# Kernel optimization log

Measured on AMD Instinct MI355X. Metric: run time of the kernel, lower is better.

The kernel has to match this reference:

```python
import jax, jax.numpy as jnp
import numpy as np

N, E, FIN, HID, TDIM, HEADS, G = 40000, 1000000, 128, 128, 16, 4, 64
C = HID // HEADS  # per-head channels = 32
NEG_SLOPE = 0.2
LN_EPS = 1e-5


def _layernorm(v, w, b):
    mu = jnp.mean(v, axis=-1, keepdims=True)
    var = jnp.var(v, axis=-1, keepdims=True)
    return (v - mu) * jax.lax.rsqrt(var + LN_EPS) * w + b


def _gat(h, src, dst, w, att_s, att_d, bias):
    # h: [N, Din]; w: [HEADS*C, Din]; att_s/att_d: [HEADS, C]
    xh = (h @ w.T).reshape(N, HEADS, C)                      # [N, HEADS, C]
    a_src = jnp.sum(xh * att_s, axis=-1)                     # [N, HEADS]
    a_dst = jnp.sum(xh * att_d, axis=-1)                     # [N, HEADS]
    e = a_src[src] + a_dst[dst]                              # [E2, HEADS]
    e = jnp.where(e > 0, e, NEG_SLOPE * e)                   # leaky_relu
    m = jax.ops.segment_max(e, dst, num_segments=N)          # [N, HEADS]
    e = jnp.exp(e - jax.lax.stop_gradient(m)[dst])
    denom = jax.ops.segment_sum(e, dst, num_segments=N)      # [N, HEADS]
    alpha = e / denom[dst]                                   # softmax over in-edges
    msg = xh[src] * alpha[..., None]                         # [E2, HEADS, C]
    out = jax.ops.segment_sum(msg, dst, num_segments=N)      # [N, HEADS, C]
    return out.reshape(N, HEADS * C) + bias


def setup_inputs() -> dict:
    key = jax.random.key(0)
    ks = jax.random.split(key, 24)
    s = lambda d: 1.0 / np.sqrt(d)
    inp = {
        "x": jax.random.normal(ks[0], (N, FIN), jnp.float32),
        "edge_index": jax.random.randint(ks[1], (2, E), 0, N, jnp.int64),
        "timestamps": jax.random.uniform(ks[2], (E,), jnp.float32) * 100.0,
        "batch": (jnp.arange(N, dtype=jnp.int64) * G) // N,
        "time_w": jax.random.normal(ks[3], (TDIM, 1), jnp.float32),
        "time_b": jax.random.normal(ks[4], (TDIM,), jnp.float32) * 0.1,
        "proj_w": jax.random.normal(ks[5], (HID, FIN), jnp.float32) * s(FIN),
        "proj_b": jnp.zeros((HID,), jnp.float32),
        "gat0_w": jax.random.normal(ks[6], (HEADS * C, HID + TDIM), jnp.float32) * s(HID + TDIM),
        "att_src0": jax.random.normal(ks[7], (HEADS, C), jnp.float32) * s(C),
        "att_dst0": jax.random.normal(ks[8], (HEADS, C), jnp.float32) * s(C),
        "gat0_b": jnp.zeros((HID,), jnp.float32),
        "ln0_w": jnp.ones((HID,), jnp.float32),
        "ln0_b": jnp.zeros((HID,), jnp.float32),
        "gat1_w": jax.random.normal(ks[9], (HEADS * C, HID), jnp.float32) * s(HID),
        "att_src1": jax.random.normal(ks[10], (HEADS, C), jnp.float32) * s(C),
        "att_dst1": jax.random.normal(ks[11], (HEADS, C), jnp.float32) * s(C),
        "gat1_b": jnp.zeros((HID,), jnp.float32),
        "ln1_w": jnp.ones((HID,), jnp.float32),
        "ln1_b": jnp.zeros((HID,), jnp.float32),
        "cls_w1": jax.random.normal(ks[12], (HID, 2 * HID), jnp.float32) * s(2 * HID),
        "cls_b1": jnp.zeros((HID,), jnp.float32),
        "cls_w2": jax.random.normal(ks[13], (2, HID), jnp.float32) * s(HID),
        "cls_b2": jnp.zeros((2,), jnp.float32),
    }
    return inp


def reference(x, edge_index, timestamps, batch, time_w, time_b, proj_w, proj_b,
              gat0_w, att_src0, att_dst0, gat0_b, ln0_w, ln0_b,
              gat1_w, att_src1, att_dst1, gat1_b, ln1_w, ln1_b,
              cls_w1, cls_b1, cls_w2, cls_b2):
    src, dst = edge_index[0], edge_index[1]
    # node projection + time-encoding scatter-add onto targets
    h = x @ proj_w.T + proj_b                                # [N, HID]
    t_enc = jnp.cos(timestamps[:, None] * time_w[:, 0] + time_b)  # [E, TDIM]
    t_node = jnp.zeros((N, TDIM), h.dtype).at[dst].add(t_enc)
    h = jnp.concatenate([h, t_node], axis=-1)                # [N, HID+TDIM]
    # add self-loops (PyG GATConv default)
    loop = jnp.arange(N, dtype=src.dtype)
    src2 = jnp.concatenate([src, loop])
    dst2 = jnp.concatenate([dst, loop])
    # layer 0 and layer 1: GAT -> LayerNorm -> ReLU (dropout off in eval)
    h = jax.nn.relu(_layernorm(_gat(h, src2, dst2, gat0_w, att_src0, att_dst0, gat0_b), ln0_w, ln0_b))
    h = jax.nn.relu(_layernorm(_gat(h, src2, dst2, gat1_w, att_src1, att_dst1, gat1_b), ln1_w, ln1_b))
    # graph pooling
    cnt = jax.ops.segment_sum(jnp.ones((N, 1), h.dtype), batch, num_segments=G)
    h_mean = jax.ops.segment_sum(h, batch, num_segments=G) / cnt
    h_max = jax.ops.segment_max(h, batch, num_segments=G)
    hg = jnp.concatenate([h_mean, h_max], axis=-1)           # [G, 2*HID]
    hg = jax.nn.relu(hg @ cls_w1.T + cls_b1)
    return hg @ cls_w2.T + cls_b2                            # [G, 2]
```

## Files before the change

### kernel.cpp

```cpp
#include <hip/hip_runtime.h>
#include <math.h>

static constexpr int kN     = 40000;
static constexpr int kE     = 1000000;
static constexpr int kTDIM  = 16;
static constexpr int kG     = 64;
static constexpr int kPOOLC = 16;
static constexpr int kNB    = (kN + 255) / 256;
static constexpr int kCH    = 2048;
static constexpr int kPB    = (kE + kCH - 1) / kCH;
#define LN_EPS 1e-5f
#define NEG_SLOPE 0.2f

typedef __attribute__((ext_vector_type(8))) short bf16x8;
typedef __attribute__((ext_vector_type(4))) float f32x4;

__device__ __forceinline__ float leaky(float v) {
  return fmaxf(v, NEG_SLOPE * v);
}

__device__ __forceinline__ unsigned short f2bf(float f) {
  unsigned u = __float_as_uint(f);
  unsigned r = u + 0x7fffu + ((u >> 16) & 1u);
  return (unsigned short)(r >> 16);
}
__device__ __forceinline__ float bflo(unsigned u) { return __uint_as_float(u << 16); }
__device__ __forceinline__ float bfhi(unsigned u) { return __uint_as_float(u & 0xffff0000u); }

static constexpr int kP0 = 256 * 128;
static constexpr int kP1 = kP0 + 128 * 128;
static constexpr int kP2 = kP1 + 128 * 160;
static constexpr int kP3 = kP2 + 128 * 128;
static constexpr int kP4 = kP3 + kNB;
__global__ void __launch_bounds__(256) k_prep(
    const float* __restrict__ c1w, float* __restrict__ c1T,
    const float* __restrict__ pw, unsigned short* __restrict__ pwb,
    const float* __restrict__ g0w, unsigned short* __restrict__ w0b,
    const float* __restrict__ g1w, unsigned short* __restrict__ w1b,
    int* __restrict__ gbhist) {
  int idx = blockIdx.x * 256 + threadIdx.x;
  if (idx < kP0) {
    int j = idx / 256, k = idx - j * 256;
    c1T[k * 128 + j] = c1w[idx];
  } else if (idx < kP1) {
    int i = idx - kP0;
    pwb[i] = f2bf(pw[i]);
  } else if (idx < kP2) {
    int i = idx - kP1;
    int j = i / 160, k = i - j * 160;
    w0b[i] = (k < 144) ? f2bf(g0w[j * 144 + k]) : (unsigned short)0;
  } else if (idx < kP3) {
    int i = idx - kP2;
    w1b[i] = f2bf(g1w[i]);
  } else if (idx < kP4) {
    gbhist[idx - kP3] = 0;
  }
}

__global__ void __launch_bounds__(256) k_part0(const int* __restrict__ dst,
                                               int* __restrict__ gbhist) {
  __shared__ int h[kNB];
  int t = threadIdx.x;
  for (int i = t; i < kNB; i += 256) h[i] = 0;
  __syncthreads();
  int base = blockIdx.x * kCH;
#pragma unroll
  for (int i = 0; i < kCH / 256; ++i) {
    int e = base + i * 256 + t;
    if (e < kE) atomicAdd(&h[dst[e] >> 8], 1);
  }
  __syncthreads();
  for (int i = t; i < kNB; i += 256) {
    int c = h[i];
    if (c) atomicAdd(gbhist + i, c);
  }
}

__global__ void __launch_bounds__(256) k_bprefix(const int* __restrict__ gbhist,
                                                 int* __restrict__ bucketbase,
                                                 int* __restrict__ gcursor,
                                                 int* __restrict__ rowptr) {
  __shared__ int sh[256];
  int t = threadIdx.x;
  int v = (t < kNB) ? gbhist[t] : 0;
  sh[t] = v;
  __syncthreads();
  for (int off = 1; off < 256; off <<= 1) {
    int a = (t >= off) ? sh[t - off] : 0;
    __syncthreads();
    sh[t] += a;
    __syncthreads();
  }
  int excl = sh[t] - v;
  if (t <= kNB) bucketbase[t] = excl;
  if (t < kNB) gcursor[t] = excl;
  if (t == 0) rowptr[kN] = kE;
}

__global__ void __launch_bounds__(256) k_part1(
    const int* __restrict__ src, const int* __restrict__ dst,
    const float* __restrict__ ts, int* __restrict__ gcursor,
    unsigned long long* __restrict__ tmp) {
  __shared__ int hist[kNB];
  __shared__ int lbase[kNB];
  int t = threadIdx.x;
  for (int i = t; i < kNB; i += 256) hist[i] = 0;
  __syncthreads();
  int base = blockIdx.x * kCH;
  int bk[8];
  unsigned long long ent[8];
#pragma unroll
  for (int i = 0; i < 8; ++i) {
    int e = base + i * 256 + t;
    if (e < kE) {
      int d = dst[e];
      int b = d >> 8;
      bk[i] = b;
      unsigned lo = (unsigned)src[e] | ((unsigned)(d & 255) << 16);
      ent[i] = ((unsigned long long)(unsigned)__float_as_int(ts[e]) << 32) | lo;
      atomicAdd(&hist[b], 1);
    } else {
      bk[i] = -1;
    }
  }
  __syncthreads();
  for (int i = t; i < kNB; i += 256) {
    int c = hist[i];
    lbase[i] = c ? atomicAdd(gcursor + i, c) : 0;
  }
  __syncthreads();
  for (int i = t; i < kNB; i += 256) hist[i] = 0;
  __syncthreads();
#pragma unroll
  for (int i = 0; i < 8; ++i) {
    if (bk[i] >= 0) {
      int off = atomicAdd(&hist[bk[i]], 1);
      tmp[lbase[bk[i]] + off] = ent[i];
    }
  }
}

__global__ void __launch_bounds__(256) k_part2(
    const unsigned long long* __restrict__ tmp, const int* __restrict__ bucketbase,
    int* __restrict__ rowptr, int2* __restrict__ csr) {
  __shared__ int cnt[256];
  __shared__ int sh[256];
  __shared__ int cur[256];
  int b = blockIdx.x;
  int t = threadIdx.x;
  int lo = bucketbase[b], hi = bucketbase[b + 1];
  int nnode = kN - b * 256;
  nnode = nnode < 256 ? nnode : 256;
  cnt[t] = 0;
  __syncthreads();
  for (int p = lo + t; p < hi; p += 256)
    atomicAdd(&cnt[((unsigned)tmp[p] >> 16) & 255], 1);
  __syncthreads();
  int v = cnt[t];
  sh[t] = v;
  __syncthreads();
  for (int off = 1; off < 256; off <<= 1) {
    int a = (t >= off) ? sh[t - off] : 0;
    __syncthreads();
    sh[t] += a;
    __syncthreads();
  }
  int nodebase = lo + sh[t] - v;
  if (t < nnode) rowptr[b * 256 + t] = nodebase;
  cur[t] = nodebase;
  __syncthreads();
  for (int p = lo + t; p < hi; p += 256) {
    unsigned long long e = tmp[p];
    unsigned elo = (unsigned)e;
    int pos = atomicAdd(&cur[(elo >> 16) & 255], 1);
    csr[pos] = make_int2((int)(elo & 0xffffu), (int)(unsigned)(e >> 32));
  }
}

__global__ void __launch_bounds__(256) k_time_gather(
    const int* __restrict__ rowptr, const int2* __restrict__ csr,
    const float* __restrict__ tw, const float* __restrict__ tb,
    unsigned short* __restrict__ hb) {
  int n = blockIdx.x * 4 + (threadIdx.x >> 6);
  if (n >= kN) return;
  int lane = threadIdx.x & 63;
  int j = lane & 15, grp = lane >> 4;
  float w = tw[j], b = tb[j];
  int lo = rowptr[n], hi = rowptr[n + 1];
  float s = 0.f;
  for (int p = lo + grp; p < hi; p += 4) {
    s += cosf(__int_as_float(csr[p].y) * w + b);
  }
  s += __shfl_xor(s, 16);
  s += __shfl_xor(s, 32);
  if (grp == 0) hb[(size_t)n * 160 + 128 + j] = f2bf(s);
  if (grp == 1) hb[(size_t)n * 160 + 144 + j] = 0;
}

__global__ void __launch_bounds__(256) k_mfma_proj(
    const float* __restrict__ x, const unsigned short* __restrict__ wb,
    const float* __restrict__ bias, unsigned short* __restrict__ outb) {
  int n0 = blockIdx.x * 16;
  int wv = threadIdx.x >> 6, l = threadIdx.x & 63;
  int lr = l & 15, lk = l >> 4;
  const int K = 128;
  int jt0 = 2 * wv, jt1 = 2 * wv + 1;
  const float* arow = x + (size_t)(n0 + lr) * K + lk * 8;
  const unsigned short* brow0 = wb + (size_t)(jt0 * 16 + lr) * K + lk * 8;
  const unsigned short* brow1 = wb + (size_t)(jt1 * 16 + lr) * K + lk * 8;
  f32x4 acc0 = {0.f, 0.f, 0.f, 0.f}, acc1 = {0.f, 0.f, 0.f, 0.f};
#pragma unroll
  for (int c = 0; c < 4; ++c) {
    float4 alo = *(const float4*)(arow + c * 32);
    float4 ahi = *(const float4*)(arow + c * 32 + 4);
    bf16x8 a;
    a[0] = (short)f2bf(alo.x); a[1] = (short)f2bf(alo.y);
    a[2] = (short)f2bf(alo.z); a[3] = (short)f2bf(alo.w);
    a[4] = (short)f2bf(ahi.x); a[5] = (short)f2bf(ahi.y);
    a[6] = (short)f2bf(ahi.z); a[7] = (short)f2bf(ahi.w);
    acc0 = __builtin_amdgcn_mfma_f32_16x16x32_bf16(a, *(const bf16x8*)(brow0 + c * 32), acc0, 0, 0, 0);
    acc1 = __builtin_amdgcn_mfma_f32_16x16x32_bf16(a, *(const bf16x8*)(brow1 + c * 32), acc1, 0, 0, 0);
  }
  int j0 = jt0 * 16 + lr, j1 = jt1 * 16 + lr;
  float bb0 = bias[j0], bb1 = bias[j1];
#pragma unroll
  for (int r = 0; r < 4; ++r) {
    int node = n0 + lk * 4 + r;
    outb[(size_t)node * 160 + j0] = f2bf(acc0[r] + bb0);
    outb[(size_t)node * 160 + j1] = f2bf(acc1[r] + bb1);
  }
}

__global__ void __launch_bounds__(256) k_mfma_xh_att(
    const unsigned short* __restrict__ hb, int K,
    const unsigned short* __restrict__ wb,
    const float* __restrict__ att_s, const float* __restrict__ att_d,
    unsigned short* __restrict__ xh, float* __restrict__ a_src,
    float* __restrict__ a_dst) {
  int n0 = blockIdx.x * 16;
  int wv = threadIdx.x >> 6, l = threadIdx.x & 63;
  int lr = l & 15, lk = l >> 4;
  int jt0 = 2 * wv, jt1 = 2 * wv + 1;
  const unsigned short* arow = hb + (size_t)(n0 + lr) * K + lk * 8;
  const unsigned short* brow0 = wb + (size_t)(jt0 * 16 + lr) * K + lk * 8;
  const unsigned short* brow1 = wb + (size_t)(jt1 * 16 + lr) * K + lk * 8;
  f32x4 acc0 = {0.f, 0.f, 0.f, 0.f}, acc1 = {0.f, 0.f, 0.f, 0.f};
  int nch = K >> 5;
  for (int c = 0; c < nch; ++c) {
    bf16x8 a = *(const bf16x8*)(arow + c * 32);
    acc0 = __builtin_amdgcn_mfma_f32_16x16x32_bf16(a, *(const bf16x8*)(brow0 + c * 32), acc0, 0, 0, 0);
    acc1 = __builtin_amdgcn_mfma_f32_16x16x32_bf16(a, *(const bf16x8*)(brow1 + c * 32), acc1, 0, 0, 0);
  }
  int j0 = jt0 * 16 + lr, j1 = jt1 * 16 + lr;
  float as0 = att_s[j0], as1 = att_s[j1];
  float ad0 = att_d[j0], ad1 = att_d[j1];
#pragma unroll
  for (int r = 0; r < 4; ++r) {
    int node = n0 + lk * 4 + r;
    float d0 = acc0[r], d1 = acc1[r];
    xh[(size_t)node * 128 + j0] = f2bf(d0);
    xh[(size_t)node * 128 + j1] = f2bf(d1);
    float vs = d0 * as0 + d1 * as1;
    float vd = d0 * ad0 + d1 * ad1;
    vs += __shfl_xor(vs, 1); vs += __shfl_xor(vs, 2);
    vs += __shfl_xor(vs, 4); vs += __shfl_xor(vs, 8);
    vd += __shfl_xor(vd, 1); vd += __shfl_xor(vd, 2);
    vd += __shfl_xor(vd, 4); vd += __shfl_xor(vd, 8);
    if (lr == 0) {
      a_src[node * 4 + wv] = vs;
      a_dst[node * 4 + wv] = vd;
    }
  }
}

__global__ void __launch_bounds__(256) k_gat_agg(
    const unsigned short* __restrict__ xh, const float* __restrict__ a_src,
    const float* __restrict__ a_dst,
    const int* __restrict__ rowptr, const int2* __restrict__ csr,
    const float* __restrict__ gb, const float* __restrict__ lw,
    const float* __restrict__ lb, unsigned short* __restrict__ outb) {
  int n = blockIdx.x * 4 + (threadIdx.x >> 6);
  if (n >= kN) return;
  int lane = threadIdx.x & 63;
  int eg = lane >> 4;
  int li = lane & 15;
  int hd = li >> 2;
  float ad = a_dst[n * 4 + hd];
  const int* csrx = (const int*)csr;

  float den = 0.f;
  float a0 = 0.f, a1 = 0.f, a2 = 0.f, a3 = 0.f, a4 = 0.f, a5 = 0.f, a6 = 0.f, a7 = 0.f;

  if (eg == 0) {
    float w_self = __expf(leaky(a_src[n * 4 + hd] + ad));
    den = w_self;
    uint4 u = ((const uint4*)(xh + (size_t)n * 128))[li];
    a0 = w_self * bflo(u.x); a1 = w_self * bfhi(u.x);
    a2 = w_self * bflo(u.y); a3 = w_self * bfhi(u.y);
    a4 = w_self * bflo(u.z); a5 = w_self * bfhi(u.z);
    a6 = w_self * bflo(u.w); a7 = w_self * bfhi(u.w);
  }

  int lo = rowptr[n], hi = rowptr[n + 1];
  int s_cur = -1;
  uint4 u_cur = {0, 0, 0, 0};
  float asrc_cur = 0.f;
  {
    int e = lo + eg;
    if (e < hi) {
      s_cur = csrx[2 * (size_t)e];
      u_cur = ((const uint4*)(xh + (size_t)s_cur * 128))[li];
      asrc_cur = a_src[s_cur * 4 + hd];
    }
  }
  for (int p = lo; p < hi; p += 4) {
    int s_next = -1;
    uint4 u_next = {0, 0, 0, 0};
    float asrc_next = 0.f;
    int en = p + 4 + eg;
    if (en < hi) {
      s_next = csrx[2 * (size_t)en];
      u_next = ((const uint4*)(xh + (size_t)s_next * 128))[li];
      asrc_next = a_src[s_next * 4 + hd];
    }
    if (s_cur >= 0) {
      float wv = __expf(leaky(asrc_cur + ad));
      den += wv;
      a0 += wv * bflo(u_cur.x); a1 += wv * bfhi(u_cur.x);
      a2 += wv * bflo(u_cur.y); a3 += wv * bfhi(u_cur.y);
      a4 += wv * bflo(u_cur.z); a5 += wv * bfhi(u_cur.z);
      a6 += wv * bflo(u_cur.w); a7 += wv * bfhi(u_cur.w);
    }
    s_cur = s_next;
    u_cur = u_next;
    asrc_cur = asrc_next;
  }

#pragma unroll
  for (int off = 16; off <= 32; off <<= 1) {
    den += __shfl_xor(den, off);
    a0 += __shfl_xor(a0, off); a1 += __shfl_xor(a1, off);
    a2 += __shfl_xor(a2, off); a3 += __shfl_xor(a3, off);
    a4 += __shfl_xor(a4, off); a5 += __shfl_xor(a5, off);
    a6 += __shfl_xor(a6, off); a7 += __shfl_xor(a7, off);
  }

  float inv = 1.f / den;
  int c0 = li * 8;
  float4 gbl = *(const float4*)(gb + c0);
  float4 gbh = *(const float4*)(gb + c0 + 4);
  float v0 = a0 * inv + gbl.x, v1 = a1 * inv + gbl.y;
  float v2 = a2 * inv + gbl.z, v3 = a3 * inv + gbl.w;
  float v4 = a4 * inv + gbh.x, v5 = a5 * inv + gbh.y;
  float v6 = a6 * inv + gbh.z, v7 = a7 * inv + gbh.w;
  float s = v0 + v1 + v2 + v3 + v4 + v5 + v6 + v7;
  float sq = v0*v0 + v1*v1 + v2*v2 + v3*v3 + v4*v4 + v5*v5 + v6*v6 + v7*v7;
#pragma unroll
  for (int off = 1; off <= 8; off <<= 1) {
    s += __shfl_xor(s, off);
    sq += __shfl_xor(sq, off);
  }
  float mean = s * (1.f / 128.f);
  float var = sq * (1.f / 128.f) - mean * mean;
  float rs = rsqrtf(var + LN_EPS);
  if (eg == 0) {
    float4 lwl = *(const float4*)(lw + c0), lwh = *(const float4*)(lw + c0 + 4);
    float4 lbl = *(const float4*)(lb + c0), lbh = *(const float4*)(lb + c0 + 4);
    float y0 = fmaxf((v0 - mean) * rs * lwl.x + lbl.x, 0.f);
    float y1 = fmaxf((v1 - mean) * rs * lwl.y + lbl.y, 0.f);
    float y2 = fmaxf((v2 - mean) * rs * lwl.z + lbl.z, 0.f);
    float y3 = fmaxf((v3 - mean) * rs * lwl.w + lbl.w, 0.f);
    float y4 = fmaxf((v4 - mean) * rs * lwh.x + lbh.x, 0.f);
    float y5 = fmaxf((v5 - mean) * rs * lwh.y + lbh.y, 0.f);
    float y6 = fmaxf((v6 - mean) * rs * lwh.z + lbh.z, 0.f);
    float y7 = fmaxf((v7 - mean) * rs * lwh.w + lbh.w, 0.f);
    uint4 o;
    o.x = (unsigned)f2bf(y0) | ((unsigned)f2bf(y1) << 16);
    o.y = (unsigned)f2bf(y2) | ((unsigned)f2bf(y3) << 16);
    o.z = (unsigned)f2bf(y4) | ((unsigned)f2bf(y5) << 16);
    o.w = (unsigned)f2bf(y6) | ((unsigned)f2bf(y7) << 16);
    *(uint4*)(outb + (size_t)n * 128 + c0) = o;
  }
}

__global__ void __launch_bounds__(128) k_pool1(
    const unsigned short* __restrict__ h, const int* __restrict__ batch,
    float* __restrict__ psum, float* __restrict__ pmax) {
  int g = blockIdx.x >> 4, chunk = blockIdx.x & (kPOOLC - 1);
  int c = threadIdx.x;
  int lo, hi;
  { int a = 0, b = kN; while (a < b) { int m = (a + b) >> 1; if (batch[m] < g) a = m + 1; else b = m; } lo = a; }
  { int a = 0, b = kN; while (a < b) { int m = (a + b) >> 1; if (batch[m] < g + 1) a = m + 1; else b = m; } hi = a; }
  int len = hi - lo;
  int c0 = lo + (int)(((long long)len * chunk) / kPOOLC);
  int c1 = lo + (int)(((long long)len * (chunk + 1)) / kPOOLC);
  float s = 0.f, mx = -INFINITY;
  for (int n = c0; n < c1; ++n) {
    float v = __uint_as_float(((unsigned)h[(size_t)n * 128 + c]) << 16);
    s += v;
    mx = fmaxf(mx, v);
  }
  psum[(size_t)blockIdx.x * 128 + c] = s;
  pmax[(size_t)blockIdx.x * 128 + c] = mx;
}

__global__ void __launch_bounds__(128) k_pool2_cls(
    const float* __restrict__ psum, const float* __restrict__ pmax,
    const int* __restrict__ batch,
    const float* __restrict__ w1t, const float* __restrict__ b1,
    const float* __restrict__ w2, const float* __restrict__ b2,
    float* __restrict__ out) {
  __shared__ float row[256];
  __shared__ float o1[128];
  int g = blockIdx.x;
  int c = threadIdx.x;
  int lo, hi;
  { int a = 0, b = kN; while (a < b) { int m = (a + b) >> 1; if (batch[m] < g) a = m + 1; else b = m; } lo = a; }
  { int a = 0, b = kN; while (a < b) { int m = (a + b) >> 1; if (batch[m] < g + 1) a = m + 1; else b = m; } hi = a; }
  float s = 0.f, mx = -INFINITY;
#pragma unroll
  for (int k = 0; k < kPOOLC; ++k) {
    s += psum[(size_t)(g * kPOOLC + k) * 128 + c];
    mx = fmaxf(mx, pmax[(size_t)(g * kPOOLC + k) * 128 + c]);
  }
  int cnt = hi - lo;
  row[c] = (cnt > 0) ? s / (float)cnt : 0.f;
  row[c + 128] = mx;
  __syncthreads();
  float t = b1[c];
  for (int k = 0; k < 256; ++k) t += row[k] * w1t[k * 128 + c];
  o1[c] = fmaxf(t, 0.f);
  __syncthreads();
  if (c < 2) {
    float r = b2[c];
    for (int j = 0; j < 128; ++j) r += o1[j] * w2[c * 128 + j];
    out[g * 2 + c] = r;
  }
}

extern "C" void kernel_launch(void* const* d_in, const int* in_sizes, int n_in,
                              void* d_out, int out_size, void* d_ws, size_t ws_size,
                              hipStream_t stream) {
  const float* x      = (const float*)d_in[0];
  const int*   ei     = (const int*)d_in[1];
  const float* ts     = (const float*)d_in[2];
  const int*   batch  = (const int*)d_in[3];
  const float* time_w = (const float*)d_in[4];
  const float* time_b = (const float*)d_in[5];
  const float* proj_w = (const float*)d_in[6];
  const float* proj_b = (const float*)d_in[7];
  const float* g0w    = (const float*)d_in[8];
  const float* as0    = (const float*)d_in[9];
  const float* ad0    = (const float*)d_in[10];
  const float* g0b    = (const float*)d_in[11];
  const float* ln0w   = (const float*)d_in[12];
  const float* ln0b   = (const float*)d_in[13];
  const float* g1w    = (const float*)d_in[14];
  const float* as1    = (const float*)d_in[15];
  const float* ad1    = (const float*)d_in[16];
  const float* g1b    = (const float*)d_in[17];
  const float* ln1w   = (const float*)d_in[18];
  const float* ln1b   = (const float*)d_in[19];
  const float* c1w    = (const float*)d_in[20];
  const float* c1b    = (const float*)d_in[21];
  const float* c2w    = (const float*)d_in[22];
  const float* c2b    = (const float*)d_in[23];
  float* out = (float*)d_out;

  const int* src = ei;
  const int* dst = ei + kE;

  char* p = (char*)d_ws;
  unsigned short* xh   = (unsigned short*)p; p += (size_t)kN * 128 * 2;
  unsigned short* hb16 = (unsigned short*)p; p += (size_t)kN * 160 * 2;
  unsigned short* h1b16= (unsigned short*)p; p += (size_t)kN * 128 * 2;
  float* a_src = (float*)p; p += (size_t)kN * 4 * 4;
  float* a_dst = (float*)p; p += (size_t)kN * 4 * 4;
  unsigned short* pwb = (unsigned short*)p; p += 128 * 128 * 2;
  unsigned short* w0b = (unsigned short*)p; p += 128 * 160 * 2;
  unsigned short* w1b = (unsigned short*)p; p += 128 * 128 * 2;
  float* c1T = (float*)p; p += 256 * 128 * 4;
  int2* csr = (int2*)p; p += (size_t)kE * 8;
  unsigned long long* tmp = (unsigned long long*)p; p += (size_t)kE * 8;
  float* psum = (float*)p; p += (size_t)kG * kPOOLC * 128 * 4;
  float* pmax = (float*)p; p += (size_t)kG * kPOOLC * 128 * 4;
  int* rowptr = (int*)p; p += (kN + 1) * 4;
  int* gbhist = (int*)p; p += kNB * 4;
  int* bucketbase = (int*)p; p += (kNB + 1) * 4;
  int* gcursor = (int*)p; p += kNB * 4;

  k_prep<<<(kP4 + 255) / 256, 256, 0, stream>>>(c1w, c1T, proj_w, pwb, g0w, w0b,
                                                g1w, w1b, gbhist);

  k_part0<<<kPB, 256, 0, stream>>>(dst, gbhist);
  k_bprefix<<<1, 256, 0, stream>>>(gbhist, bucketbase, gcursor, rowptr);
  k_part1<<<kPB, 256, 0, stream>>>(src, dst, ts, gcursor, tmp);
  k_part2<<<kNB, 256, 0, stream>>>(tmp, bucketbase, rowptr, csr);

  k_mfma_proj<<<kN / 16, 256, 0, stream>>>(x, pwb, proj_b, hb16);
  k_time_gather<<<kN / 4, 256, 0, stream>>>(rowptr, csr, time_w, time_b, hb16);

  k_mfma_xh_att<<<kN / 16, 256, 0, stream>>>(hb16, 160, w0b, as0, ad0, xh, a_src, a_dst);
  k_gat_agg<<<kN / 4, 256, 0, stream>>>(xh, a_src, a_dst, rowptr, csr,
                                        g0b, ln0w, ln0b, h1b16);

  k_mfma_xh_att<<<kN / 16, 256, 0, stream>>>(h1b16, 128, w1b, as1, ad1, xh, a_src, a_dst);
  k_gat_agg<<<kN / 4, 256, 0, stream>>>(xh, a_src, a_dst, rowptr, csr,
                                        g1b, ln1w, ln1b, h1b16);

  k_pool1<<<kG * kPOOLC, 128, 0, stream>>>(h1b16, batch, psum, pmax);
  k_pool2_cls<<<kG, 128, 0, stream>>>(psum, pmax, batch, c1T, c1b, c2w, c2b, out);
}
```

Before: 270.8 us.

## Split CSR into separate src/ts arrays, fuse histogram into prep, double chunk size

Splits the interleaved int2 CSR (src, timestamp) into two separate arrays. The GAT aggregation kernels now read only the src indices and the time gather reads only timestamps, which halves the bytes each pass touches. It also folds the dst histogram kernel into the weight-prep kernel, zeroing the histogram with a memset, and doubles the partition chunk size so fewer blocks contend on global atomics. The larger chunks mean more registers per thread in the partition kernel and fewer blocks to spread across the GPU.

```diff
diff --git a/kernel.cpp b/kernel.cpp
--- a/kernel.cpp
+++ b/kernel.cpp
@@ -7,7 +7,7 @@
 static constexpr int kG     = 64;
 static constexpr int kPOOLC = 16;
 static constexpr int kNB    = (kN + 255) / 256;
-static constexpr int kCH    = 2048;
+static constexpr int kCH    = 4096;
 static constexpr int kPB    = (kE + kCH - 1) / kCH;
 #define LN_EPS 1e-5f
 #define NEG_SLOPE 0.2f
@@ -31,14 +31,33 @@
 static constexpr int kP1 = kP0 + 128 * 128;
 static constexpr int kP2 = kP1 + 128 * 160;
 static constexpr int kP3 = kP2 + 128 * 128;
-static constexpr int kP4 = kP3 + kNB;
+static constexpr int kPREPB = (kP3 + 255) / 256;
 __global__ void __launch_bounds__(256) k_prep(
+    const int* __restrict__ dst, int* __restrict__ gbhist,
     const float* __restrict__ c1w, float* __restrict__ c1T,
     const float* __restrict__ pw, unsigned short* __restrict__ pwb,
     const float* __restrict__ g0w, unsigned short* __restrict__ w0b,
-    const float* __restrict__ g1w, unsigned short* __restrict__ w1b,
-    int* __restrict__ gbhist) {
-  int idx = blockIdx.x * 256 + threadIdx.x;
+    const float* __restrict__ g1w, unsigned short* __restrict__ w1b) {
+  int b = blockIdx.x;
+  int t = threadIdx.x;
+  if (b < kPB) {
+    __shared__ int h[kNB];
+    for (int i = t; i < kNB; i += 256) h[i] = 0;
+    __syncthreads();
+    int base = b * kCH;
+#pragma unroll
+    for (int i = 0; i < kCH / 256; ++i) {
+      int e = base + i * 256 + t;
+      if (e < kE) atomicAdd(&h[dst[e] >> 8], 1);
+    }
+    __syncthreads();
+    for (int i = t; i < kNB; i += 256) {
+      int c = h[i];
+      if (c) atomicAdd(gbhist + i, c);
+    }
+    return;
+  }
+  int idx = (b - kPB) * 256 + t;
   if (idx < kP0) {
     int j = idx / 256, k = idx - j * 256;
     c1T[k * 128 + j] = c1w[idx];
@@ -52,27 +71,6 @@
   } else if (idx < kP3) {
     int i = idx - kP2;
     w1b[i] = f2bf(g1w[i]);
-  } else if (idx < kP4) {
-    gbhist[idx - kP3] = 0;
-  }
-}
-
-__global__ void __launch_bounds__(256) k_part0(const int* __restrict__ dst,
-                                               int* __restrict__ gbhist) {
-  __shared__ int h[kNB];
-  int t = threadIdx.x;
-  for (int i = t; i < kNB; i += 256) h[i] = 0;
-  __syncthreads();
-  int base = blockIdx.x * kCH;
-#pragma unroll
-  for (int i = 0; i < kCH / 256; ++i) {
-    int e = base + i * 256 + t;
-    if (e < kE) atomicAdd(&h[dst[e] >> 8], 1);
-  }
-  __syncthreads();
-  for (int i = t; i < kNB; i += 256) {
-    int c = h[i];
-    if (c) atomicAdd(gbhist + i, c);
   }
 }
 
@@ -107,10 +105,10 @@
   for (int i = t; i < kNB; i += 256) hist[i] = 0;
   __syncthreads();
   int base = blockIdx.x * kCH;
-  int bk[8];
-  unsigned long long ent[8];
-#pragma unroll
-  for (int i = 0; i < 8; ++i) {
+  int bk[kCH / 256];
+  unsigned long long ent[kCH / 256];
+#pragma unroll
+  for (int i = 0; i < kCH / 256; ++i) {
     int e = base + i * 256 + t;
     if (e < kE) {
       int d = dst[e];
@@ -132,7 +130,7 @@
   for (int i = t; i < kNB; i += 256) hist[i] = 0;
   __syncthreads();
 #pragma unroll
-  for (int i = 0; i < 8; ++i) {
+  for (int i = 0; i < kCH / 256; ++i) {
     if (bk[i] >= 0) {
       int off = atomicAdd(&hist[bk[i]], 1);
       tmp[lbase[bk[i]] + off] = ent[i];
@@ -142,7 +140,8 @@
 
 __global__ void __launch_bounds__(256) k_part2(
     const unsigned long long* __restrict__ tmp, const int* __restrict__ bucketbase,
-    int* __restrict__ rowptr, int2* __restrict__ csr) {
+    int* __restrict__ rowptr, int* __restrict__ csr_src,
+    float* __restrict__ csr_ts) {
   __shared__ int cnt[256];
   __shared__ int sh[256];
   __shared__ int cur[256];
@@ -173,12 +172,13 @@
     unsigned long long e = tmp[p];
     unsigned elo = (unsigned)e;
     int pos = atomicAdd(&cur[(elo >> 16) & 255], 1);
-    csr[pos] = make_int2((int)(elo & 0xffffu), (int)(unsigned)(e >> 32));
+    csr_src[pos] = (int)(elo & 0xffffu);
+    csr_ts[pos] = __uint_as_float((unsigned)(e >> 32));
   }
 }
 
 __global__ void __launch_bounds__(256) k_time_gather(
-    const int* __restrict__ rowptr, const int2* __restrict__ csr,
+    const int* __restrict__ rowptr, const float* __restrict__ csr_ts,
     const float* __restrict__ tw, const float* __restrict__ tb,
     unsigned short* __restrict__ hb) {
   int n = blockIdx.x * 4 + (threadIdx.x >> 6);
@@ -189,7 +189,7 @@
   int lo = rowptr[n], hi = rowptr[n + 1];
   float s = 0.f;
   for (int p = lo + grp; p < hi; p += 4) {
-    s += cosf(__int_as_float(csr[p].y) * w + b);
+    s += cosf(csr_ts[p] * w + b);
   }
   s += __shfl_xor(s, 16);
   s += __shfl_xor(s, 32);
@@ -276,7 +276,7 @@
 __global__ void __launch_bounds__(256) k_gat_agg(
     const unsigned short* __restrict__ xh, const float* __restrict__ a_src,
     const float* __restrict__ a_dst,
-    const int* __restrict__ rowptr, const int2* __restrict__ csr,
+    const int* __restrict__ rowptr, const int* __restrict__ csr_src,
     const float* __restrict__ gb, const float* __restrict__ lw,
     const float* __restrict__ lb, unsigned short* __restrict__ outb) {
   int n = blockIdx.x * 4 + (threadIdx.x >> 6);
@@ -286,7 +286,6 @@
   int li = lane & 15;
   int hd = li >> 2;
   float ad = a_dst[n * 4 + hd];
-  const int* csrx = (const int*)csr;
 
   float den = 0.f;
   float a0 = 0.f, a1 = 0.f, a2 = 0.f, a3 = 0.f, a4 = 0.f, a5 = 0.f, a6 = 0.f, a7 = 0.f;
@@ -308,7 +307,7 @@
   {
     int e = lo + eg;
     if (e < hi) {
-      s_cur = csrx[2 * (size_t)e];
+      s_cur = csr_src[e];
       u_cur = ((const uint4*)(xh + (size_t)s_cur * 128))[li];
       asrc_cur = a_src[s_cur * 4 + hd];
     }
@@ -319,7 +318,7 @@
     float asrc_next = 0.f;
     int en = p + 4 + eg;
     if (en < hi) {
-      s_next = csrx[2 * (size_t)en];
+      s_next = csr_src[en];
       u_next = ((const uint4*)(xh + (size_t)s_next * 128))[li];
       asrc_next = a_src[s_next * 4 + hd];
     }
@@ -480,7 +479,8 @@
   unsigned short* w0b = (unsigned short*)p; p += 128 * 160 * 2;
   unsigned short* w1b = (unsigned short*)p; p += 128 * 128 * 2;
   float* c1T = (float*)p; p += 256 * 128 * 4;
-  int2* csr = (int2*)p; p += (size_t)kE * 8;
+  int* csr_src = (int*)p; p += (size_t)kE * 4;
+  float* csr_ts = (float*)p; p += (size_t)kE * 4;
   unsigned long long* tmp = (unsigned long long*)p; p += (size_t)kE * 8;
   float* psum = (float*)p; p += (size_t)kG * kPOOLC * 128 * 4;
   float* pmax = (float*)p; p += (size_t)kG * kPOOLC * 128 * 4;
@@ -489,23 +489,23 @@
   int* bucketbase = (int*)p; p += (kNB + 1) * 4;
   int* gcursor = (int*)p; p += kNB * 4;
 
-  k_prep<<<(kP4 + 255) / 256, 256, 0, stream>>>(c1w, c1T, proj_w, pwb, g0w, w0b,
-                                                g1w, w1b, gbhist);
-
-  k_part0<<<kPB, 256, 0, stream>>>(dst, gbhist);
+  hipMemsetAsync(gbhist, 0, kNB * sizeof(int), stream);
+  k_prep<<<kPB + kPREPB, 256, 0, stream>>>(dst, gbhist, c1w, c1T, proj_w, pwb,
+                                           g0w, w0b, g1w, w1b);
+
   k_bprefix<<<1, 256, 0, stream>>>(gbhist, bucketbase, gcursor, rowptr);
   k_part1<<<kPB, 256, 0, stream>>>(src, dst, ts, gcursor, tmp);
-  k_part2<<<kNB, 256, 0, stream>>>(tmp, bucketbase, rowptr, csr);
+  k_part2<<<kNB, 256, 0, stream>>>(tmp, bucketbase, rowptr, csr_src, csr_ts);
 
   k_mfma_proj<<<kN / 16, 256, 0, stream>>>(x, pwb, proj_b, hb16);
-  k_time_gather<<<kN / 4, 256, 0, stream>>>(rowptr, csr, time_w, time_b, hb16);
+  k_time_gather<<<kN / 4, 256, 0, stream>>>(rowptr, csr_ts, time_w, time_b, hb16);
 
   k_mfma_xh_att<<<kN / 16, 256, 0, stream>>>(hb16, 160, w0b, as0, ad0, xh, a_src, a_dst);
-  k_gat_agg<<<kN / 4, 256, 0, stream>>>(xh, a_src, a_dst, rowptr, csr,
+  k_gat_agg<<<kN / 4, 256, 0, stream>>>(xh, a_src, a_dst, rowptr, csr_src,
                                         g0b, ln0w, ln0b, h1b16);
 
   k_mfma_xh_att<<<kN / 16, 256, 0, stream>>>(h1b16, 128, w1b, as1, ad1, xh, a_src, a_dst);
-  k_gat_agg<<<kN / 4, 256, 0, stream>>>(xh, a_src, a_dst, rowptr, csr,
+  k_gat_agg<<<kN / 4, 256, 0, stream>>>(xh, a_src, a_dst, rowptr, csr_src,
                                         g1b, ln1w, ln1b, h1b16);
 
   k_pool1<<<kG * kPOOLC, 128, 0, stream>>>(h1b16, batch, psum, pmax);
```

Result: no change. 268.6 us (-0.8%).
